# Performance work log

Hardware: AMD Instinct MI355X
Metric: run time of the kernel (lower is better)

Reference implementation:

```python
import jax, jax.numpy as jnp
import numpy as np

BATCH, CHANNELS, SIZE = 64, 256, 4096

def setup_inputs() -> dict:
    key = jax.random.key(0)
    k1, k2, k3 = jax.random.split(key, 3)
    x = jax.random.normal(k1, (BATCH, CHANNELS, SIZE), dtype=jnp.float32)
    # xavier_uniform-style scale for weights (fan_in=channels, fan_out=size)
    limit = float(np.sqrt(6.0 / (CHANNELS + SIZE)))
    weights = jax.random.uniform(k2, (CHANNELS, SIZE), dtype=jnp.float32, minval=-limit, maxval=limit)
    bias = jnp.zeros((SIZE,), dtype=jnp.float32)
    return {"x": x, "weights": weights, "bias": bias}

def capped_relu(x):
    # pass through values in (0, 1], zero elsewhere
    return jnp.where((x > 0) & (x <= 1), x, jnp.zeros_like(x))

def reference(x, weights, bias):
    # diag(sample.T @ W)[i] == sum_c x[b,c,i] * W[c,i]  -> channel-wise dot product
    out = jnp.einsum('bcs,cs->bs', x, weights) + bias  # [B, size]
    return capped_relu(out)  # node_activation=True
```

## Files before the change

### kernel.cpp

```cpp
#include <hip/hip_runtime.h>


#define BATCH    64
#define CHANNELS 256
#define SIZE     4096

__device__ __forceinline__ float capped_relu(float v) {
    return (v > 0.0f && v <= 1.0f) ? v : 0.0f;
}

__global__ __launch_bounds__(256) void CWG_30794915512765_kernel(
    const float* __restrict__ x,
    const float* __restrict__ w,
    const float* __restrict__ bias,
    float* __restrict__ out)
{
    const int bid = blockIdx.x;
    const int b   = bid >> 2;
    const int s   = ((bid & 3) << 10) + (threadIdx.x << 2);

    const float* xcol = x + (size_t)b * CHANNELS * SIZE + s;
    const float* wcol = w + s;

    float4 acc = make_float4(0.0f, 0.0f, 0.0f, 0.0f);

#pragma unroll 8
    for (int c = 0; c < CHANNELS; ++c) {
        const float4 xv = *reinterpret_cast<const float4*>(xcol + (size_t)c * SIZE);
        const float4 wv = *reinterpret_cast<const float4*>(wcol + (size_t)c * SIZE);
        acc.x += xv.x * wv.x;
        acc.y += xv.y * wv.y;
        acc.z += xv.z * wv.z;
        acc.w += xv.w * wv.w;
    }

    const float4 bv = *reinterpret_cast<const float4*>(bias + s);
    float4 o;
    o.x = capped_relu(acc.x + bv.x);
    o.y = capped_relu(acc.y + bv.y);
    o.z = capped_relu(acc.z + bv.z);
    o.w = capped_relu(acc.w + bv.w);

    *reinterpret_cast<float4*>(out + (size_t)b * SIZE + s) = o;
}

extern "C" void kernel_launch(void* const* d_in, const int* in_sizes, int n_in,
                              void* d_out, int out_size, void* d_ws, size_t ws_size,
                              hipStream_t stream) {
    const float* x    = (const float*)d_in[0];
    const float* w    = (const float*)d_in[1];
    const float* bias = (const float*)d_in[2];
    float* out        = (float*)d_out;

    const int blocks = BATCH * (SIZE / 1024);
    CWG_30794915512765_kernel<<<blocks, 256, 0, stream>>>(x, w, bias, out);
}
```

Before: 354.7 us.

## Split channel reduction across thread groups with shared-memory combine

After: 358.6 us. About the same (+1.1%).

```diff
diff --git a/kernel.cpp b/kernel.cpp
--- a/kernel.cpp
+++ b/kernel.cpp
@@ -5,43 +5,65 @@
 #define CHANNELS 256
 #define SIZE     4096
 
+#define CG   4
+#define TS   512
+#define TPG  (TS / 4)
+#define TPB  (CG * TPG)
+#define CPG  (CHANNELS / CG)
+#define NTILE (SIZE / TS)
+
 __device__ __forceinline__ float capped_relu(float v) {
     return (v > 0.0f && v <= 1.0f) ? v : 0.0f;
 }
 
-__global__ __launch_bounds__(256) void CWG_30794915512765_kernel(
+__global__ __launch_bounds__(TPB) void CWG_30794915512765_kernel(
     const float* __restrict__ x,
     const float* __restrict__ w,
     const float* __restrict__ bias,
     float* __restrict__ out)
 {
+    __shared__ float4 part[CG - 1][TPG];
+
+    const int tid = threadIdx.x;
+    const int g   = tid >> 7;
+    const int t   = tid & (TPG - 1);
     const int bid = blockIdx.x;
-    const int b   = bid >> 2;
-    const int s   = ((bid & 3) << 10) + (threadIdx.x << 2);
+    const int b     = bid >> 3;
+    const int stile = bid & (NTILE - 1);
+    const int s     = stile * TS + (t << 2);
 
-    const float* xcol = x + (size_t)b * CHANNELS * SIZE + s;
-    const float* wcol = w + s;
+    const float* xp = x + (size_t)b * CHANNELS * SIZE + (size_t)g * CPG * SIZE + s;
+    const float* wp = w + (size_t)g * CPG * SIZE + s;
 
     float4 acc = make_float4(0.0f, 0.0f, 0.0f, 0.0f);
 
 #pragma unroll 8
-    for (int c = 0; c < CHANNELS; ++c) {
-        const float4 xv = *reinterpret_cast<const float4*>(xcol + (size_t)c * SIZE);
-        const float4 wv = *reinterpret_cast<const float4*>(wcol + (size_t)c * SIZE);
+    for (int c = 0; c < CPG; ++c) {
+        const float4 xv = *reinterpret_cast<const float4*>(xp + (size_t)c * SIZE);
+        const float4 wv = *reinterpret_cast<const float4*>(wp + (size_t)c * SIZE);
         acc.x += xv.x * wv.x;
         acc.y += xv.y * wv.y;
         acc.z += xv.z * wv.z;
         acc.w += xv.w * wv.w;
     }
 
-    const float4 bv = *reinterpret_cast<const float4*>(bias + s);
-    float4 o;
-    o.x = capped_relu(acc.x + bv.x);
-    o.y = capped_relu(acc.y + bv.y);
-    o.z = capped_relu(acc.z + bv.z);
-    o.w = capped_relu(acc.w + bv.w);
+    if (g != 0) part[g - 1][t] = acc;
+    __syncthreads();
 
-    *reinterpret_cast<float4*>(out + (size_t)b * SIZE + s) = o;
+    if (g == 0) {
+#pragma unroll
+        for (int k = 0; k < CG - 1; ++k) {
+            const float4 p = part[k][t];
+            acc.x += p.x; acc.y += p.y; acc.z += p.z; acc.w += p.w;
+        }
+        const float4 bv = *reinterpret_cast<const float4*>(bias + s);
+        float4 o;
+        o.x = capped_relu(acc.x + bv.x);
+        o.y = capped_relu(acc.y + bv.y);
+        o.z = capped_relu(acc.z + bv.z);
+        o.w = capped_relu(acc.w + bv.w);
+        *reinterpret_cast<float4*>(out + (size_t)b * SIZE + s) = o;
+    }
 }
 
 extern "C" void kernel_launch(void* const* d_in, const int* in_sizes, int n_in,
@@ -52,6 +74,6 @@
     const float* bias = (const float*)d_in[2];
     float* out        = (float*)d_out;
 
-    const int blocks = BATCH * (SIZE / 1024);
-    CWG_30794915512765_kernel<<<blocks, 256, 0, stream>>>(x, w, bias, out);
+    const int blocks = BATCH * NTILE;
+    CWG_30794915512765_kernel<<<blocks, TPB, 0, stream>>>(x, w, bias, out);
 }
```
